# Optimization experiments

Measured on AMD Instinct MI355X. Metric: run time of the kernel, lower is better.

The kernel has to match this reference:

```python
import jax, jax.numpy as jnp
import numpy as np

N, E, R = 50000, 500000, 3
IN, HID, OUT = 128, 128, 128
NEG_SLOPE = 0.2


def setup_inputs() -> dict:
    key = jax.random.key(0)
    ks = jax.random.split(key, 16)
    g = lambda i, shape: jax.random.normal(ks[i], shape, jnp.float32) * 0.1
    return {
        "x": jax.random.normal(ks[0], (N, IN), jnp.float32),
        "edge_index": jax.random.randint(ks[1], (2, E), 0, N, jnp.int32),
        "edge_type": jax.random.randint(ks[2], (E,), 0, R, jnp.int32),
        "edge_attr": jax.random.normal(ks[3], (E, 1), jnp.float32),
        # conv1 params (RGATConv: per-relation weight, q/k/e attention vectors, edge lin, bias)
        "w1": g(4, (R, IN, HID)), "q1": g(5, (HID, 1)), "k1": g(6, (HID, 1)),
        "le1": g(7, (1, HID)), "e1": g(8, (HID, 1)), "b1": jnp.zeros((HID,), jnp.float32),
        # conv2 params
        "w2": g(9, (R, HID, OUT)), "q2": g(10, (OUT, 1)), "k2": g(11, (OUT, 1)),
        "le2": g(12, (1, OUT)), "e2": g(13, (OUT, 1)), "b2": jnp.zeros((OUT,), jnp.float32),
    }


def _rgat_conv(x, src, dst, edge_type, edge_attr, w, q, k, le, e, b):
    """PyG RGATConv: heads=1, dim=1, additive-self-attention, across-relation softmax."""
    n = x.shape[0]
    # Per-relation linear at node level (equiv. to per-edge bmm with w[edge_type])
    xw = jnp.einsum('ni,rio->rno', x, w)            # [R, N, C]
    x_j = xw[edge_type, src]                          # [E, C] transformed source feats
    x_i = xw[edge_type, dst]                          # [E, C] transformed target feats
    # additive attention logits: q(x_i) + k(x_j) + e(lin_edge(edge_attr))
    alpha = x_i @ q + x_j @ k + (edge_attr @ le) @ e  # [E, 1]
    alpha = jax.nn.leaky_relu(alpha, negative_slope=NEG_SLOPE)
    # across-relation softmax over incoming edges of each target node
    amax = jax.ops.segment_max(alpha, dst, num_segments=n)
    amax = jnp.where(jnp.isfinite(amax), amax, 0.0)   # empty segments -> 0
    ex = jnp.exp(alpha - amax[dst])
    denom = jax.ops.segment_sum(ex, dst, num_segments=n)
    alpha = ex / (denom[dst] + 1e-16)
    # weighted scatter-add aggregation, then bias (concat=True, heads=1)
    out = jax.ops.segment_sum(alpha * x_j, dst, num_segments=n)  # [N, C]
    return out + b


def reference(x, edge_index, edge_type, edge_attr,
              w1, q1, k1, le1, e1, b1,
              w2, q2, k2, le2, e2, b2):
    src, dst = edge_index[0], edge_index[1]
    h = jax.nn.relu(_rgat_conv(x, src, dst, edge_type, edge_attr, w1, q1, k1, le1, e1, b1))
    return _rgat_conv(h, src, dst, edge_type, edge_attr, w2, q2, k2, le2, e2, b2)
```

## Files before the change

kernel.cpp:

```cpp
#include <hip/hip_runtime.h>
#include <hip/hip_bf16.h>
#include <math.h>

typedef __bf16 bf16x8 __attribute__((ext_vector_type(8)));
typedef float f32x4 __attribute__((ext_vector_type(4)));

#define CDIM 128

__global__ void sentinel_kernel(float* outf) {
  if (threadIdx.x == 0) outf[0] = 12345.0f;
}

__global__ __launch_bounds__(256) void prep_kernel(
    const float* __restrict__ w1, const float* __restrict__ w2,
    __hip_bfloat16* __restrict__ wt,
    const float* __restrict__ le1, const float* __restrict__ e1,
    const float* __restrict__ le2, const float* __restrict__ e2,
    float* __restrict__ outc, int* __restrict__ deg, int perW, int n) {
  const int b = blockIdx.x;
  const int tid = threadIdx.x;
  if (b < 48) {
    int t = b * 256 + tid;
    if (t >= perW * 2) return;
    const float* w = (t < perW) ? w1 : w2;
    int tt = (t < perW) ? t : t - perW;
    int r = tt >> 11;
    int rem = tt & 2047;
    int kb = rem >> 7;
    int o = rem & 127;
    const float* wr = w + ((size_t)r << 14);
    union { __hip_bfloat16 h[8]; int4 v; } u;
#pragma unroll
    for (int j = 0; j < 8; ++j)
      u.h[j] = __float2bfloat16(wr[(size_t)(kb * 8 + j) * CDIM + o]);
    *reinterpret_cast<int4*>(wt + (size_t)t * 8) = u.v;
  } else if (b == 48) {
    if (tid < 64) {
      float v1 = le1[tid] * e1[tid] + le1[tid + 64] * e1[tid + 64];
      float v2 = le2[tid] * e2[tid] + le2[tid + 64] * e2[tid + 64];
#pragma unroll
      for (int off = 32; off > 0; off >>= 1) {
        v1 += __shfl_xor(v1, off, 64);
        v2 += __shfl_xor(v2, off, 64);
      }
      if (tid == 0) { outc[0] = v1; outc[1] = v2; }
    }
  } else {
    int i = (b - 49) * 256 + tid;
    if (i < n) deg[i] = 0;
  }
}


__global__ __launch_bounds__(256) void hist_kernel(const int* __restrict__ dstv,
                                                   int* __restrict__ deg, int E) {
  int e = blockIdx.x * 256 + threadIdx.x;
  if (e < E) atomicAdd(&deg[dstv[e]], 1);
}

__global__ __launch_bounds__(256) void scan1_kernel(const int* __restrict__ deg,
                                                    int* __restrict__ rowptr,
                                                    int* __restrict__ partials, int n) {
  __shared__ int sh[256];
  int t = threadIdx.x;
  int base = blockIdx.x * 1024;
  int idx = base + t * 4;
  int v[4]; int s = 0;
#pragma unroll
  for (int j = 0; j < 4; ++j) { v[j] = (idx + j < n) ? deg[idx + j] : 0; s += v[j]; }
  sh[t] = s;
  __syncthreads();
  for (int off = 1; off < 256; off <<= 1) {
    int x = (t >= off) ? sh[t - off] : 0;
    __syncthreads();
    sh[t] += x;
    __syncthreads();
  }
  int excl = sh[t] - s;
  if (t == 255) partials[blockIdx.x] = sh[255];
  int run = excl;
#pragma unroll
  for (int j = 0; j < 4; ++j) {
    if (idx + j < n) rowptr[idx + j] = run;
    run += v[j];
  }
}

__global__ __launch_bounds__(256) void scan2_kernel(int* __restrict__ partials, int nb) {
  __shared__ int sh[256];
  int t = threadIdx.x;
  int v = (t < nb) ? partials[t] : 0;
  sh[t] = v;
  __syncthreads();
  for (int off = 1; off < 256; off <<= 1) {
    int x = (t >= off) ? sh[t - off] : 0;
    __syncthreads();
    sh[t] += x;
    __syncthreads();
  }
  if (t < nb) partials[t] = sh[t] - v;
}

__global__ __launch_bounds__(256) void scan3_kernel(int* __restrict__ rowptr,
                                                    int* __restrict__ cursor,
                                                    const int* __restrict__ partials,
                                                    int n, int E) {
  int i = blockIdx.x * 256 + threadIdx.x;
  if (i < n) {
    int v = rowptr[i] + partials[i >> 10];
    rowptr[i] = v;
    cursor[i] = v;
  } else if (i == n) {
    rowptr[n] = E;
  }
}

__global__ __launch_bounds__(256) void scatter_kernel(
    const int* __restrict__ srcv, const int* __restrict__ dstv,
    const int* __restrict__ etype, const float* __restrict__ eattr,
    int* __restrict__ cursor, int2* __restrict__ kattr, int E, int n) {
  int e = blockIdx.x * 256 + threadIdx.x;
  if (e >= E) return;
  int p = atomicAdd(&cursor[dstv[e]], 1);
  kattr[p] = make_int2(etype[e] * n + srcv[e], __float_as_int(eattr[e]));
}

__global__ __launch_bounds__(256) void gemm_xw_kernel(
    const float* __restrict__ xin, const __hip_bfloat16* __restrict__ wt,
    const float* __restrict__ qv, const float* __restrict__ kv,
    __hip_bfloat16* __restrict__ xwout, float* __restrict__ sq, float* __restrict__ sk,
    int n) {
  __shared__ __hip_bfloat16 wlds[16 * 128 * 8];
  const int base = blockIdx.x * 128;
  const int tid = threadIdx.x;
  const int wave = tid >> 6, lane = tid & 63;
  const int quad = lane >> 4, c16 = lane & 15;

  bf16x8 zf;
#pragma unroll
  for (int j = 0; j < 8; ++j) zf[j] = (__bf16)0.0f;

  bf16x8 af[2][4];
#pragma unroll
  for (int h = 0; h < 2; ++h) {
    int m = base + wave * 32 + h * 16 + c16;
#pragma unroll
    for (int ks = 0; ks < 4; ++ks) {
      if (m < n) {
        const float* xp = xin + (size_t)m * CDIM + ks * 32 + quad * 8;
        f32x4 x0 = *reinterpret_cast<const f32x4*>(xp);
        f32x4 x1 = *reinterpret_cast<const f32x4*>(xp + 4);
        bf16x8 a;
#pragma unroll
        for (int j = 0; j < 4; ++j) { a[j] = (__bf16)x0[j]; a[4 + j] = (__bf16)x1[j]; }
        af[h][ks] = a;
      } else {
        af[h][ks] = zf;
      }
    }
  }

  float qf[8], kf[8];
#pragma unroll
  for (int nt = 0; nt < 8; ++nt) {
    qf[nt] = qv[nt * 16 + c16];
    kf[nt] = kv[nt * 16 + c16];
  }

  for (int r = 0; r < 3; ++r) {
    if (r) __syncthreads();
    {
      const int4* src = reinterpret_cast<const int4*>(wt + ((size_t)r << 14));
      int4* dst = reinterpret_cast<int4*>(wlds);
      for (int i = tid; i < 2048; i += 256) dst[i] = src[i];
    }
    __syncthreads();

    f32x4 acc[2][8];
#pragma unroll
    for (int h = 0; h < 2; ++h)
#pragma unroll
      for (int nt = 0; nt < 8; ++nt) acc[h][nt] = (f32x4){0.f, 0.f, 0.f, 0.f};

#pragma unroll
    for (int ks = 0; ks < 4; ++ks) {
#pragma unroll
      for (int nt = 0; nt < 8; ++nt) {
        bf16x8 b = *reinterpret_cast<const bf16x8*>(
            &wlds[(((ks * 4 + quad) * 128) + nt * 16 + c16) * 8]);
        acc[0][nt] = __builtin_amdgcn_mfma_f32_16x16x32_bf16(af[0][ks], b, acc[0][nt], 0, 0, 0);
        acc[1][nt] = __builtin_amdgcn_mfma_f32_16x16x32_bf16(af[1][ks], b, acc[1][nt], 0, 0, 0);
      }
    }

#pragma unroll
    for (int h = 0; h < 2; ++h) {
      int rowb = base + wave * 32 + h * 16 + quad * 4;
#pragma unroll
      for (int reg = 0; reg < 4; ++reg) {
        int grow = rowb + reg;
        float s_q = 0.f, s_k = 0.f;
#pragma unroll
        for (int nt = 0; nt < 8; ++nt) {
          float v = acc[h][nt][reg];
          if (grow < n)
            xwout[(((size_t)r * n + grow) << 7) + nt * 16 + c16] = __float2bfloat16(v);
          s_q += v * qf[nt];
          s_k += v * kf[nt];
        }
#pragma unroll
        for (int off = 1; off < 16; off <<= 1) {
          s_q += __shfl_xor(s_q, off, 64);
          s_k += __shfl_xor(s_k, off, 64);
        }
        if (c16 == 0 && grow < n) {
          sq[r * n + grow] = s_q;
          sk[r * n + grow] = s_k;
        }
      }
    }
  }
}

__global__ __launch_bounds__(256) void aggregate_kernel(
    const int* __restrict__ rowptr, const int2* __restrict__ kattr,
    const float* __restrict__ sq, const float* __restrict__ sk,
    const __hip_bfloat16* __restrict__ xw, const float* __restrict__ bias,
    const float* __restrict__ cscal, float* __restrict__ out, int n, int do_relu) {
  const int wave = threadIdx.x >> 6, lane = threadIdx.x & 63;
  const int node = blockIdx.x * 4 + wave;
  if (node >= n) return;
  const int g = lane >> 4;
  const int sub = lane & 15;
  const float c = cscal[0];
  const int n2 = n * 2;

  const int start = rowptr[node];
  const int deg = rowptr[node + 1] - start;
  const float s0 = sq[node], s1 = sq[n + node], s2 = sq[n2 + node];

  float acc[8];
#pragma unroll
  for (int t = 0; t < 8; ++t) acc[t] = 0.f;
  float den = 0.f;

  for (int j0 = 0; j0 < deg; j0 += 4) {
    int j = j0 + g;
    if (j < deg) {
      int2 ka = kattr[start + j];
      int kk = ka.x;
      float sv = (kk >= n2) ? s2 : ((kk >= n) ? s1 : s0);
      float l = sv + sk[kk] + c * __int_as_float(ka.y);
      l = l > 0.f ? l : 0.2f * l;
      float w = __expf(l);
      bf16x8 f = *reinterpret_cast<const bf16x8*>(xw + ((size_t)kk << 7) + sub * 8);
#pragma unroll
      for (int t = 0; t < 8; ++t) acc[t] += w * (float)f[t];
      den += w;
    }
  }

#pragma unroll
  for (int t = 0; t < 8; ++t) {
    acc[t] += __shfl_xor(acc[t], 16, 64);
    acc[t] += __shfl_xor(acc[t], 32, 64);
  }
  den += __shfl_xor(den, 16, 64);
  den += __shfl_xor(den, 32, 64);

  if (g == 0) {
    float inv = 1.0f / (den + 1e-16f);
    f32x4 b0 = *reinterpret_cast<const f32x4*>(bias + sub * 8);
    f32x4 b1 = *reinterpret_cast<const f32x4*>(bias + sub * 8 + 4);
    f32x4 o0, o1;
#pragma unroll
    for (int t = 0; t < 4; ++t) {
      o0[t] = acc[t] * inv + b0[t];
      o1[t] = acc[4 + t] * inv + b1[t];
    }
    if (do_relu) {
#pragma unroll
      for (int t = 0; t < 4; ++t) {
        o0[t] = fmaxf(o0[t], 0.f);
        o1[t] = fmaxf(o1[t], 0.f);
      }
    }
    float* op = out + (size_t)node * CDIM + sub * 8;
    *reinterpret_cast<f32x4*>(op) = o0;
    *reinterpret_cast<f32x4*>(op + 4) = o1;
  }
}


extern "C" void kernel_launch(void* const* d_in, const int* in_sizes, int n_in,
                              void* d_out, int out_size, void* d_ws, size_t ws_size,
                              hipStream_t stream) {
  const float* x     = (const float*)d_in[0];
  const int*   eidx  = (const int*)d_in[1];
  const int*   etype = (const int*)d_in[2];
  const float* eattr = (const float*)d_in[3];
  const float* w1  = (const float*)d_in[4];
  const float* q1  = (const float*)d_in[5];
  const float* k1  = (const float*)d_in[6];
  const float* le1 = (const float*)d_in[7];
  const float* e1  = (const float*)d_in[8];
  const float* b1  = (const float*)d_in[9];
  const float* w2  = (const float*)d_in[10];
  const float* q2  = (const float*)d_in[11];
  const float* k2  = (const float*)d_in[12];
  const float* le2 = (const float*)d_in[13];
  const float* e2  = (const float*)d_in[14];
  const float* b2  = (const float*)d_in[15];

  const int N = in_sizes[0] / CDIM;
  const int E = in_sizes[2];
  const int R = in_sizes[4] / (CDIM * CDIM);
  const int* srcv = eidx;
  const int* dstv = eidx + E;

  char* p = (char*)d_ws;
  auto alloc = [&](size_t bytes) -> void* {
    void* q = (void*)p;
    p += (bytes + 255) & ~(size_t)255;
    return q;
  };
  float* sq       = (float*)alloc((size_t)R * N * 4);
  float* sk       = (float*)alloc((size_t)R * N * 4);
  int*   deg      = (int*)alloc((size_t)N * 4);
  int*   rowptr   = (int*)alloc((size_t)(N + 1) * 4);
  int*   cursor   = (int*)alloc((size_t)N * 4);
  int*   partials = (int*)alloc(4096);
  int2*  kattr    = (int2*)alloc((size_t)E * 8);
  __hip_bfloat16* wt = (__hip_bfloat16*)alloc((size_t)2 * R * CDIM * CDIM * 2);
  float* cscal    = (float*)alloc(256);
  __hip_bfloat16* xw = (__hip_bfloat16*)alloc((size_t)R * N * CDIM * 2);

  size_t needed = (size_t)(p - (char*)d_ws);
  if (needed > ws_size) {
    sentinel_kernel<<<1, 64, 0, stream>>>((float*)d_out);
    return;
  }

  float* outp = (float*)d_out;
  float* hbuf = outp;

  const int eg = (E + 255) / 256;
  const int nb = (N + 1023) / 1024;
  const int nodes4 = (N + 3) / 4;
  const int perW = R * 2048;
  const int prep_grid = 49 + (N + 255) / 256;

  prep_kernel<<<prep_grid, 256, 0, stream>>>(w1, w2, wt, le1, e1, le2, e2,
                                             cscal, deg, perW, N);

  hist_kernel<<<eg, 256, 0, stream>>>(dstv, deg, E);
  scan1_kernel<<<nb, 256, 0, stream>>>(deg, rowptr, partials, N);
  scan2_kernel<<<1, 256, 0, stream>>>(partials, nb);
  scan3_kernel<<<(N + 1 + 255) / 256, 256, 0, stream>>>(rowptr, cursor, partials, N, E);
  scatter_kernel<<<eg, 256, 0, stream>>>(srcv, dstv, etype, eattr, cursor, kattr, E, N);

  dim3 ggrid((N + 127) / 128);

  gemm_xw_kernel<<<ggrid, 256, 0, stream>>>(x, wt, q1, k1, xw, sq, sk, N);
  aggregate_kernel<<<nodes4, 256, 0, stream>>>(rowptr, kattr, sq, sk, xw, b1,
                                               cscal + 0, hbuf, N, 1);

  gemm_xw_kernel<<<ggrid, 256, 0, stream>>>(hbuf, wt + (size_t)R * CDIM * CDIM,
                                            q2, k2, xw, sq, sk, N);
  aggregate_kernel<<<nodes4, 256, 0, stream>>>(rowptr, kattr, sq, sk, xw, b2,
                                               cscal + 1, outp, N, 0);
}
```

Measured before the change: 270.0 us.

## Transpose MFMA operands for vectorized xw stores and unroll edge gathers by two

The GEMM swaps the MFMA A/B operands so each lane holds four consecutive output columns of one row. That allows packed 8-byte bf16 stores and a q/k dot product whose reduction needs only two shuffles, replacing per-element stores and a 16-lane butterfly per row. The q/k vectors are now staged in shared memory. The aggregate loop handles two edges per lane-group per iteration, issuing two independent gathers to raise memory-level parallelism, at the cost of redundant loads for masked tail edges.

```diff
diff --git a/kernel.cpp b/kernel.cpp
--- a/kernel.cpp
+++ b/kernel.cpp
@@ -131,10 +131,14 @@
     __hip_bfloat16* __restrict__ xwout, float* __restrict__ sq, float* __restrict__ sk,
     int n) {
   __shared__ __hip_bfloat16 wlds[16 * 128 * 8];
+  __shared__ float qls[128], kls[128];
   const int base = blockIdx.x * 128;
   const int tid = threadIdx.x;
   const int wave = tid >> 6, lane = tid & 63;
   const int quad = lane >> 4, c16 = lane & 15;
+
+  if (tid < 128) qls[tid] = qv[tid];
+  else kls[tid - 128] = kv[tid - 128];
 
   bf16x8 zf;
 #pragma unroll
@@ -160,13 +164,6 @@
     }
   }
 
-  float qf[8], kf[8];
-#pragma unroll
-  for (int nt = 0; nt < 8; ++nt) {
-    qf[nt] = qv[nt * 16 + c16];
-    kf[nt] = kv[nt * 16 + c16];
-  }
-
   for (int r = 0; r < 3; ++r) {
     if (r) __syncthreads();
     {
@@ -180,43 +177,46 @@
 #pragma unroll
     for (int h = 0; h < 2; ++h)
 #pragma unroll
-      for (int nt = 0; nt < 8; ++nt) acc[h][nt] = (f32x4){0.f, 0.f, 0.f, 0.f};
+      for (int ot = 0; ot < 8; ++ot) acc[h][ot] = (f32x4){0.f, 0.f, 0.f, 0.f};
 
 #pragma unroll
     for (int ks = 0; ks < 4; ++ks) {
 #pragma unroll
-      for (int nt = 0; nt < 8; ++nt) {
+      for (int ot = 0; ot < 8; ++ot) {
         bf16x8 b = *reinterpret_cast<const bf16x8*>(
-            &wlds[(((ks * 4 + quad) * 128) + nt * 16 + c16) * 8]);
-        acc[0][nt] = __builtin_amdgcn_mfma_f32_16x16x32_bf16(af[0][ks], b, acc[0][nt], 0, 0, 0);
-        acc[1][nt] = __builtin_amdgcn_mfma_f32_16x16x32_bf16(af[1][ks], b, acc[1][nt], 0, 0, 0);
+            &wlds[(((ks * 4 + quad) * 128) + ot * 16 + c16) * 8]);
+        acc[0][ot] = __builtin_amdgcn_mfma_f32_16x16x32_bf16(b, af[0][ks], acc[0][ot], 0, 0, 0);
+        acc[1][ot] = __builtin_amdgcn_mfma_f32_16x16x32_bf16(b, af[1][ks], acc[1][ot], 0, 0, 0);
       }
     }
 
 #pragma unroll
     for (int h = 0; h < 2; ++h) {
-      int rowb = base + wave * 32 + h * 16 + quad * 4;
-#pragma unroll
-      for (int reg = 0; reg < 4; ++reg) {
-        int grow = rowb + reg;
-        float s_q = 0.f, s_k = 0.f;
-#pragma unroll
-        for (int nt = 0; nt < 8; ++nt) {
-          float v = acc[h][nt][reg];
-          if (grow < n)
-            xwout[(((size_t)r * n + grow) << 7) + nt * 16 + c16] = __float2bfloat16(v);
-          s_q += v * qf[nt];
-          s_k += v * kf[nt];
+      const int grow = base + wave * 32 + h * 16 + c16;
+      const bool ok = grow < n;
+      __hip_bfloat16* rp = xwout + (((size_t)r * n + grow) << 7) + quad * 4;
+      float s_q = 0.f, s_k = 0.f;
+#pragma unroll
+      for (int ot = 0; ot < 8; ++ot) {
+        f32x4 a = acc[h][ot];
+        f32x4 q4 = *reinterpret_cast<const f32x4*>(&qls[ot * 16 + quad * 4]);
+        f32x4 k4 = *reinterpret_cast<const f32x4*>(&kls[ot * 16 + quad * 4]);
+        s_q += a[0] * q4[0] + a[1] * q4[1] + a[2] * q4[2] + a[3] * q4[3];
+        s_k += a[0] * k4[0] + a[1] * k4[1] + a[2] * k4[2] + a[3] * k4[3];
+        if (ok) {
+          union { __hip_bfloat16 b4[4]; uint2 u; } pk;
+#pragma unroll
+          for (int t = 0; t < 4; ++t) pk.b4[t] = __float2bfloat16(a[t]);
+          *reinterpret_cast<uint2*>(rp + ot * 16) = pk.u;
         }
-#pragma unroll
-        for (int off = 1; off < 16; off <<= 1) {
-          s_q += __shfl_xor(s_q, off, 64);
-          s_k += __shfl_xor(s_k, off, 64);
-        }
-        if (c16 == 0 && grow < n) {
-          sq[r * n + grow] = s_q;
-          sk[r * n + grow] = s_k;
-        }
+      }
+      s_q += __shfl_xor(s_q, 16, 64);
+      s_q += __shfl_xor(s_q, 32, 64);
+      s_k += __shfl_xor(s_k, 16, 64);
+      s_k += __shfl_xor(s_k, 32, 64);
+      if (quad == 0 && ok) {
+        sq[(size_t)r * n + grow] = s_q;
+        sk[(size_t)r * n + grow] = s_k;
       }
     }
   }
@@ -244,20 +244,23 @@
   for (int t = 0; t < 8; ++t) acc[t] = 0.f;
   float den = 0.f;
 
-  for (int j0 = 0; j0 < deg; j0 += 4) {
-    int j = j0 + g;
-    if (j < deg) {
-      int2 ka = kattr[start + j];
-      int kk = ka.x;
-      float sv = (kk >= n2) ? s2 : ((kk >= n) ? s1 : s0);
-      float l = sv + sk[kk] + c * __int_as_float(ka.y);
-      l = l > 0.f ? l : 0.2f * l;
-      float w = __expf(l);
-      bf16x8 f = *reinterpret_cast<const bf16x8*>(xw + ((size_t)kk << 7) + sub * 8);
-#pragma unroll
-      for (int t = 0; t < 8; ++t) acc[t] += w * (float)f[t];
-      den += w;
-    }
+  for (int j0 = 0; j0 < deg; j0 += 8) {
+    const int j = j0 + (g << 1);
+    const bool v0 = j < deg, v1 = j + 1 < deg;
+    int2 ka0 = kattr[start + (v0 ? j : 0)];
+    int2 ka1 = kattr[start + (v1 ? j + 1 : 0)];
+    int kk0 = ka0.x, kk1 = ka1.x;
+    float l0 = (kk0 >= n2 ? s2 : (kk0 >= n ? s1 : s0)) + sk[kk0] + c * __int_as_float(ka0.y);
+    float l1 = (kk1 >= n2 ? s2 : (kk1 >= n ? s1 : s0)) + sk[kk1] + c * __int_as_float(ka1.y);
+    l0 = l0 > 0.f ? l0 : 0.2f * l0;
+    l1 = l1 > 0.f ? l1 : 0.2f * l1;
+    float w0 = v0 ? __expf(l0) : 0.f;
+    float w1 = v1 ? __expf(l1) : 0.f;
+    bf16x8 f0 = *reinterpret_cast<const bf16x8*>(xw + ((size_t)kk0 << 7) + sub * 8);
+    bf16x8 f1 = *reinterpret_cast<const bf16x8*>(xw + ((size_t)kk1 << 7) + sub * 8);
+#pragma unroll
+    for (int t = 0; t < 8; ++t) acc[t] += w0 * (float)f0[t] + w1 * (float)f1[t];
+    den += w0 + w1;
   }
 
 #pragma unroll
```

Measured after the change: 263.1 us. -2.6%, faster.
